# Performance work log

Hardware: AMD Instinct MI355X
Metric: run time of the kernel (lower is better)

Reference implementation:

```python
import jax, jax.numpy as jnp
import numpy as np

EPS = 1e-6        # RMSNorm epsilon (LLaMA convention)
THETA = 10000.0   # RoPE base, from eqx.nn.RotaryPositionalEmbedding(head_dim, 10000)


def rms_norm(x, w):
    # x: [seq, d]; w: [d]
    var = jnp.mean(x * x, axis=-1, keepdims=True)
    return x * jax.lax.rsqrt(var + EPS) * w


def rope(x, offset):
    # x: [seq, heads, head_dim]; half-split (NeoX/equinox) rotation
    seq, _, hd = x.shape
    half = hd // 2
    inv_freq = 1.0 / (THETA ** (jnp.arange(0, half, dtype=jnp.float32) * 2.0 / hd))
    pos = jnp.arange(seq, dtype=jnp.float32) + offset
    ang = jnp.outer(pos, inv_freq)              # [seq, half]
    cos = jnp.cos(ang)[:, None, :]              # [seq, 1, half]
    sin = jnp.sin(ang)[:, None, :]
    x1, x2 = x[..., :half], x[..., half:]
    return jnp.concatenate([x1 * cos - x2 * sin, x2 * cos + x1 * sin], axis=-1)


def setup_inputs() -> dict:
    D, H, HD, S, C = 4096, 32, 128, 1024, 2048
    ks = jax.random.split(jax.random.key(0), 7)
    sc = 1.0 / np.sqrt(D).astype(np.float32)
    return {
        "xs": jax.random.normal(ks[0], (S, D), jnp.float32),
        "cache_k": jax.random.normal(ks[1], (C, H, HD), jnp.float32),
        "cache_v": jax.random.normal(ks[2], (C, H, HD), jnp.float32),
        "norm_w": jnp.ones((D,), jnp.float32),
        "wq": jax.random.normal(ks[3], (D, D), jnp.float32) * sc,
        "wk": jax.random.normal(ks[4], (D, D), jnp.float32) * sc,
        "wv": jax.random.normal(ks[5], (D, D), jnp.float32) * sc,
        "wo": jax.random.normal(ks[6], (D, D), jnp.float32) * sc,
    }


def reference(xs, cache_k, cache_v, norm_w, wq, wk, wv, wo):
    S, D = xs.shape
    C, H, HD = cache_k.shape
    xn = rms_norm(xs, norm_w)                                   # [S, D]
    # eqx.nn.Linear stores weight as [out, in]: y = x @ W.T
    q = rope((xn @ wq.T).reshape(S, H, HD), C)                  # [S, H, HD]
    k_new = rope((xn @ wk.T).reshape(S, H, HD), C)
    v_new = (xn @ wv.T).reshape(S, H, HD)
    k = jnp.concatenate([cache_k, k_new], axis=0)               # [C+S, H, HD]
    v = jnp.concatenate([cache_v, v_new], axis=0)
    scores = jnp.einsum('shd,thd->hst', q, k) / np.float32(np.sqrt(HD))
    # causal with KV cache: query i (global pos C+i) attends keys j <= C+i
    mask = jnp.arange(C + S)[None, :] <= (jnp.arange(S)[:, None] + C)
    scores = jnp.where(mask[None, :, :], scores, jnp.float32(-1e30))
    probs = jax.nn.softmax(scores, axis=-1)                     # [H, S, C+S]
    attn = jnp.einsum('hst,thd->shd', probs, v).reshape(S, D)
    return attn @ wo.T                                          # [S, D]
```

## Files before the change

kernel.cpp:

```cpp
#include <hip/hip_runtime.h>
#include <cmath>

#define S_LEN 1024
#define D_DIM 4096
#define H_NUM 32
#define HD_DIM 128
#define C_LEN 2048
#define T_LEN 3072

using u16 = unsigned short;
typedef __bf16 bf16x8 __attribute__((ext_vector_type(8)));
typedef float f32x4 __attribute__((ext_vector_type(4)));

__device__ __forceinline__ u16 f2bf(float f) {
  unsigned u = __float_as_uint(f);
  return (u16)((u + 0x7FFFu + ((u >> 16) & 1u)) >> 16);
}

__device__ __forceinline__ f32x4 mfma16(bf16x8 a, bf16x8 b, f32x4 c) {
  return __builtin_amdgcn_mfma_f32_16x16x32_bf16(a, b, c, 0, 0, 0);
}

__device__ __forceinline__ void async_cp16(const u16* g, u16* l) {
  __builtin_amdgcn_global_load_lds((const __attribute__((address_space(1))) unsigned int*)g,
                                   (__attribute__((address_space(3))) unsigned int*)l,
                                   16, 0, 0);
}

__global__ __launch_bounds__(256) void cvt_w(const float* __restrict__ src, u16* __restrict__ dst, int n4) {
  int i = blockIdx.x * 256 + threadIdx.x;
  if (i >= n4) return;
  float4 v = ((const float4*)src)[i];
  ushort4 o;
  o.x = f2bf(v.x); o.y = f2bf(v.y); o.z = f2bf(v.z); o.w = f2bf(v.w);
  ((ushort4*)dst)[i] = o;
}

__global__ __launch_bounds__(256) void rmsnorm_k(const float* __restrict__ xs, const float* __restrict__ w,
                                                 u16* __restrict__ xn) {
  int row = blockIdx.x, tid = threadIdx.x;
  const float* xr = xs + (size_t)row * D_DIM;
  float4 xv[4];
  float ss = 0.f;
#pragma unroll
  for (int g = 0; g < 4; ++g) {
    xv[g] = *(const float4*)(xr + g * 1024 + tid * 4);
    ss += xv[g].x * xv[g].x + xv[g].y * xv[g].y + xv[g].z * xv[g].z + xv[g].w * xv[g].w;
  }
#pragma unroll
  for (int m = 1; m < 64; m <<= 1) ss += __shfl_xor(ss, m);
  __shared__ float red[4];
  if ((tid & 63) == 0) red[tid >> 6] = ss;
  __syncthreads();
  float rs = rsqrtf((red[0] + red[1] + red[2] + red[3]) * (1.f / D_DIM) + 1e-6f);
  u16* xo = xn + (size_t)row * D_DIM;
#pragma unroll
  for (int g = 0; g < 4; ++g) {
    float4 wv = *(const float4*)(w + g * 1024 + tid * 4);
    ushort4 o;
    o.x = f2bf(xv[g].x * rs * wv.x);
    o.y = f2bf(xv[g].y * rs * wv.y);
    o.z = f2bf(xv[g].z * rs * wv.z);
    o.w = f2bf(xv[g].w * rs * wv.w);
    *(ushort4*)(xo + g * 1024 + tid * 4) = o;
  }
}

__global__ __launch_bounds__(256) void gemm_bt(const u16* __restrict__ A,
                                               const u16* __restrict__ B0, const u16* __restrict__ B1,
                                               const u16* __restrict__ B2,
                                               float* __restrict__ C0, float* __restrict__ C1,
                                               float* __restrict__ C2) {
  __shared__ u16 As[128 * 32];
  __shared__ u16 Bs[128 * 32];
  int tid = threadIdx.x;
  int wave = tid >> 6, lane = tid & 63, quad = lane >> 4, l15 = lane & 15;
  int wm = wave >> 1, wn = wave & 1;
  int m0 = blockIdx.y * 128, n0 = blockIdx.x * 128;
  int bz = blockIdx.z;
  const u16* Bp = (bz == 0) ? B0 : ((bz == 1) ? B1 : B2);
  float* Cp = (bz == 0) ? C0 : ((bz == 1) ? C1 : C2);

  f32x4 acc[4][4];
  const f32x4 zero4 = {0.f, 0.f, 0.f, 0.f};
#pragma unroll
  for (int mt = 0; mt < 4; ++mt)
#pragma unroll
    for (int nt = 0; nt < 4; ++nt) acc[mt][nt] = zero4;

  int ar = tid >> 2, acol = (tid & 3) * 8;
  const u16* ga0 = A + (size_t)(m0 + ar) * D_DIM + acol;
  const u16* ga1 = A + (size_t)(m0 + 64 + ar) * D_DIM + acol;
  const u16* gb0 = Bp + (size_t)(n0 + ar) * D_DIM + acol;
  const u16* gb1 = Bp + (size_t)(n0 + 64 + ar) * D_DIM + acol;
  u16* la0 = As + (wave << 9);
  u16* la1 = As + 2048 + (wave << 9);
  u16* lb0 = Bs + (wave << 9);
  u16* lb1 = Bs + 2048 + (wave << 9);

  for (int k0 = 0; k0 < D_DIM; k0 += 32) {
    __syncthreads();
    async_cp16(ga0 + k0, la0);
    async_cp16(ga1 + k0, la1);
    async_cp16(gb0 + k0, lb0);
    async_cp16(gb1 + k0, lb1);
    asm volatile("s_waitcnt vmcnt(0)" ::: "memory");
    __syncthreads();
    bf16x8 af[4], bfr[4];
#pragma unroll
    for (int mt = 0; mt < 4; ++mt)
      af[mt] = *(const bf16x8*)(As + (wm * 64 + mt * 16 + l15) * 32 + quad * 8);
#pragma unroll
    for (int nt = 0; nt < 4; ++nt)
      bfr[nt] = *(const bf16x8*)(Bs + (wn * 64 + nt * 16 + l15) * 32 + quad * 8);
#pragma unroll
    for (int mt = 0; mt < 4; ++mt)
#pragma unroll
      for (int nt = 0; nt < 4; ++nt) acc[mt][nt] = mfma16(af[mt], bfr[nt], acc[mt][nt]);
  }
#pragma unroll
  for (int mt = 0; mt < 4; ++mt)
#pragma unroll
    for (int nt = 0; nt < 4; ++nt) {
      int col = n0 + wn * 64 + nt * 16 + l15;
#pragma unroll
      for (int r = 0; r < 4; ++r) {
        int rowm = m0 + wm * 64 + mt * 16 + quad * 4 + r;
        Cp[(size_t)rowm * D_DIM + col] = acc[mt][nt][r];
      }
    }
}

__global__ __launch_bounds__(256) void rope_q_k(const float* __restrict__ qlin, u16* __restrict__ qbf) {
  int idx = blockIdx.x * 256 + threadIdx.x;
  int i = idx & 63, h = (idx >> 6) & 31, s = idx >> 11;
  size_t base = (size_t)s * D_DIM + h * HD_DIM + i;
  float x1 = qlin[base], x2 = qlin[base + 64];
  float invf = expf((float)i * -0.14391156831212790f);
  float ang = (float)(s + C_LEN) * invf;
  float sn, cs;
  sincosf(ang, &sn, &cs);
  const float sc = 0.08838834764831845f;
  qbf[base] = f2bf((x1 * cs - x2 * sn) * sc);
  qbf[base + 64] = f2bf((x2 * cs + x1 * sn) * sc);
}

__global__ __launch_bounds__(256) void rope_k_k(const float* __restrict__ klin, u16* __restrict__ kc) {
  int idx = blockIdx.x * 256 + threadIdx.x;
  int i = idx & 63, h = (idx >> 6) & 31, s = idx >> 11;
  size_t base = (size_t)s * D_DIM + h * HD_DIM + i;
  float x1 = klin[base], x2 = klin[base + 64];
  float invf = expf((float)i * -0.14391156831212790f);
  float ang = (float)(s + C_LEN) * invf;
  float sn, cs;
  sincosf(ang, &sn, &cs);
  size_t ob = ((size_t)h * T_LEN + C_LEN + s) * HD_DIM + i;
  kc[ob] = f2bf(x1 * cs - x2 * sn);
  kc[ob + 64] = f2bf(x2 * cs + x1 * sn);
}

__global__ __launch_bounds__(256) void cvt_ck(const float* __restrict__ ck, u16* __restrict__ kc) {
  int idx = blockIdx.x * 256 + threadIdx.x;
  int flat = idx * 4;
  int c = flat >> 12, h = (flat >> 7) & 31, hd = flat & 127;
  float4 v = *(const float4*)(ck + flat);
  ushort4 o;
  o.x = f2bf(v.x); o.y = f2bf(v.y); o.z = f2bf(v.z); o.w = f2bf(v.w);
  *(ushort4*)(kc + ((size_t)h * T_LEN + c) * HD_DIM + hd) = o;
}

__global__ __launch_bounds__(256) void trans_v(const float* __restrict__ src, u16* __restrict__ vt, int tofs) {
  int h = blockIdx.z, d0 = blockIdx.x * 64, r0 = blockIdx.y * 64;
  __shared__ float tile[64][65];
  int tid = threadIdx.x;
  int rr = tid >> 4, c4 = (tid & 15) * 4;
#pragma unroll
  for (int p = 0; p < 4; ++p) {
    int r = p * 16 + rr;
    float4 v = *(const float4*)(src + (size_t)(r0 + r) * D_DIM + h * HD_DIM + d0 + c4);
    tile[r][c4] = v.x; tile[r][c4 + 1] = v.y; tile[r][c4 + 2] = v.z; tile[r][c4 + 3] = v.w;
  }
  __syncthreads();
#pragma unroll
  for (int p = 0; p < 4; ++p) {
    int dl = p * 16 + rr;
    ushort4 o;
    o.x = f2bf(tile[c4 + 0][dl]);
    o.y = f2bf(tile[c4 + 1][dl]);
    o.z = f2bf(tile[c4 + 2][dl]);
    o.w = f2bf(tile[c4 + 3][dl]);
    *(ushort4*)(vt + ((size_t)h * HD_DIM + d0 + dl) * T_LEN + tofs + r0 + c4) = o;
  }
}

__global__ __launch_bounds__(256) void attn_k(const u16* __restrict__ qb, const u16* __restrict__ kc,
                                              const u16* __restrict__ vt, u16* __restrict__ ob) {
  int qt = blockIdx.x, h = blockIdx.y;
  int tid = threadIdx.x, wave = tid >> 6, lane = tid & 63, quad = lane >> 4, l15 = lane & 15;
  __shared__ u16 Ks[64 * 136];
  __shared__ u16 Vs[128 * 72];
  __shared__ u16 Ps[4 * 16 * 72];

  int qrow = qt * 64 + wave * 16 + l15;
  bf16x8 qf[4];
#pragma unroll
  for (int kt = 0; kt < 4; ++kt)
    qf[kt] = *(const bf16x8*)(qb + (size_t)qrow * D_DIM + h * HD_DIM + kt * 32 + quad * 8);

  f32x4 O[8];
  const f32x4 zero4 = {0.f, 0.f, 0.f, 0.f};
#pragma unroll
  for (int i = 0; i < 8; ++i) O[i] = zero4;
  float mrun[4] = {-INFINITY, -INFINITY, -INFINITY, -INFINITY};
  float lrun[4] = {0.f, 0.f, 0.f, 0.f};

  int ktl = tid >> 2, kcc = (tid & 3) * 32;
  int vd = tid >> 1, vtt = (tid & 1) * 32;
  const u16* kg = kc + ((size_t)h * T_LEN + ktl) * HD_DIM + kcc;
  const u16* vg = vt + ((size_t)h * HD_DIM + vd) * T_LEN + vtt;
  u16* kl = Ks + ktl * 136 + kcc;
  u16* vl = Vs + vd * 72 + vtt;

  int nkb = 33 + qt;
  for (int kb = 0; kb < nkb; ++kb) {
    __syncthreads();
#pragma unroll
    for (int u = 0; u < 4; ++u)
      *(bf16x8*)(kl + u * 8) = *(const bf16x8*)(kg + (size_t)kb * 64 * HD_DIM + u * 8);
#pragma unroll
    for (int u = 0; u < 4; ++u)
      *(bf16x8*)(vl + u * 8) = *(const bf16x8*)(vg + (size_t)kb * 64 + u * 8);
    __syncthreads();

    f32x4 sc4[4];
#pragma unroll
    for (int nt = 0; nt < 4; ++nt) {
      f32x4 s = zero4;
#pragma unroll
      for (int kt = 0; kt < 4; ++kt) {
        bf16x8 bv = *(const bf16x8*)(Ks + (nt * 16 + l15) * 136 + kt * 32 + quad * 8);
        s = mfma16(qf[kt], bv, s);
      }
      sc4[nt] = s;
    }
    if (kb == nkb - 1) {
#pragma unroll
      for (int nt = 0; nt < 4; ++nt) {
        int t = kb * 64 + nt * 16 + l15;
#pragma unroll
        for (int r = 0; r < 4; ++r) {
          int srow = qt * 64 + wave * 16 + quad * 4 + r;
          if (t > C_LEN + srow) sc4[nt][r] = -INFINITY;
        }
      }
    }
    float alpha4[4];
#pragma unroll
    for (int r = 0; r < 4; ++r) {
      float mx = fmaxf(fmaxf(sc4[0][r], sc4[1][r]), fmaxf(sc4[2][r], sc4[3][r]));
      mx = fmaxf(mx, __shfl_xor(mx, 1));
      mx = fmaxf(mx, __shfl_xor(mx, 2));
      mx = fmaxf(mx, __shfl_xor(mx, 4));
      mx = fmaxf(mx, __shfl_xor(mx, 8));
      float nm = fmaxf(mrun[r], mx);
      float al = __expf(mrun[r] - nm);
      float ps = 0.f;
#pragma unroll
      for (int nt = 0; nt < 4; ++nt) {
        float p = __expf(sc4[nt][r] - nm);
        sc4[nt][r] = p;
        ps += p;
      }
      ps += __shfl_xor(ps, 1);
      ps += __shfl_xor(ps, 2);
      ps += __shfl_xor(ps, 4);
      ps += __shfl_xor(ps, 8);
      lrun[r] = lrun[r] * al + ps;
      mrun[r] = nm;
      alpha4[r] = al;
    }
#pragma unroll
    for (int i = 0; i < 8; ++i)
#pragma unroll
      for (int r = 0; r < 4; ++r) O[i][r] *= alpha4[r];

    u16* pw = Ps + wave * (16 * 72);
#pragma unroll
    for (int nt = 0; nt < 4; ++nt)
#pragma unroll
      for (int r = 0; r < 4; ++r)
        pw[(quad * 4 + r) * 72 + nt * 16 + l15] = f2bf(sc4[nt][r]);
    asm volatile("s_waitcnt lgkmcnt(0)" ::: "memory");

#pragma unroll
    for (int kt2 = 0; kt2 < 2; ++kt2) {
      bf16x8 af = *(const bf16x8*)(pw + l15 * 72 + kt2 * 32 + quad * 8);
#pragma unroll
      for (int nt2 = 0; nt2 < 8; ++nt2) {
        bf16x8 bv = *(const bf16x8*)(Vs + (nt2 * 16 + l15) * 72 + kt2 * 32 + quad * 8);
        O[nt2] = mfma16(af, bv, O[nt2]);
      }
    }
  }
  float inv[4];
#pragma unroll
  for (int r = 0; r < 4; ++r) inv[r] = 1.f / lrun[r];
#pragma unroll
  for (int nt2 = 0; nt2 < 8; ++nt2)
#pragma unroll
    for (int r = 0; r < 4; ++r) {
      int srow = qt * 64 + wave * 16 + quad * 4 + r;
      ob[(size_t)srow * D_DIM + h * HD_DIM + nt2 * 16 + l15] = f2bf(O[nt2][r] * inv[r]);
    }
}

extern "C" void kernel_launch(void* const* d_in, const int* in_sizes, int n_in,
                              void* d_out, int out_size, void* d_ws, size_t ws_size,
                              hipStream_t stream) {
  const float* xs = (const float*)d_in[0];
  const float* cache_k = (const float*)d_in[1];
  const float* cache_v = (const float*)d_in[2];
  const float* norm_w = (const float*)d_in[3];
  const float* wq = (const float*)d_in[4];
  const float* wk = (const float*)d_in[5];
  const float* wv = (const float*)d_in[6];
  const float* wo = (const float*)d_in[7];
  float* out = (float*)d_out;

  char* ws = (char*)d_ws;
  size_t off = 0;
  auto take = [&](size_t b) -> void* {
    char* p = ws + off;
    off += (b + 255) & ~(size_t)255;
    return (void*)p;
  };
  u16* wq_bf = (u16*)take((size_t)D_DIM * D_DIM * 2);
  u16* wk_bf = (u16*)take((size_t)D_DIM * D_DIM * 2);
  u16* wv_bf = (u16*)take((size_t)D_DIM * D_DIM * 2);
  u16* wo_bf = (u16*)take((size_t)D_DIM * D_DIM * 2);
  u16* xn_bf = (u16*)take((size_t)S_LEN * D_DIM * 2);
  float* q_lin = (float*)take((size_t)S_LEN * D_DIM * 4);
  float* k_lin = (float*)take((size_t)S_LEN * D_DIM * 4);
  float* v_lin = (float*)take((size_t)S_LEN * D_DIM * 4);
  u16* q_bf = (u16*)take((size_t)S_LEN * D_DIM * 2);
  u16* k_cat = (u16*)take((size_t)H_NUM * T_LEN * HD_DIM * 2);
  u16* v_t = (u16*)take((size_t)H_NUM * T_LEN * HD_DIM * 2);
  u16* attn_bf = (u16*)take((size_t)S_LEN * D_DIM * 2);

  int n4w = D_DIM * D_DIM / 4;
  cvt_w<<<n4w / 256, 256, 0, stream>>>(wq, wq_bf, n4w);
  cvt_w<<<n4w / 256, 256, 0, stream>>>(wk, wk_bf, n4w);
  cvt_w<<<n4w / 256, 256, 0, stream>>>(wv, wv_bf, n4w);
  cvt_w<<<n4w / 256, 256, 0, stream>>>(wo, wo_bf, n4w);
  rmsnorm_k<<<S_LEN, 256, 0, stream>>>(xs, norm_w, xn_bf);
  gemm_bt<<<dim3(32, 8, 3), 256, 0, stream>>>(xn_bf, wq_bf, wk_bf, wv_bf, q_lin, k_lin, v_lin);
  rope_q_k<<<(S_LEN * H_NUM * 64) / 256, 256, 0, stream>>>(q_lin, q_bf);
  rope_k_k<<<(S_LEN * H_NUM * 64) / 256, 256, 0, stream>>>(k_lin, k_cat);
  cvt_ck<<<(C_LEN * H_NUM * HD_DIM / 4) / 256, 256, 0, stream>>>(cache_k, k_cat);
  trans_v<<<dim3(2, C_LEN / 64, H_NUM), 256, 0, stream>>>(cache_v, v_t, 0);
  trans_v<<<dim3(2, S_LEN / 64, H_NUM), 256, 0, stream>>>(v_lin, v_t, C_LEN);
  attn_k<<<dim3(16, 32), 256, 0, stream>>>(q_bf, k_cat, v_t, attn_bf);
  gemm_bt<<<dim3(32, 8, 1), 256, 0, stream>>>(attn_bf, wo_bf, wo_bf, wo_bf, out, out, out);
}
```

Before: 808.9 us.

## Double-buffer attention K/V with async loads, deepen GEMM k-step, merge small kernels

The attention kernel now stages K and V tiles into double-buffered shared memory with async global-to-LDS copies and XOR-swizzled layouts, so the next tile's loads overlap compute. The P scratch now reuses the current K buffer behind an extra barrier. The GEMM loads two 32-wide k-slices per barrier, halving the sync count. Weight conversion, RoPE and V transposition are each merged into a single launch to cut launch overhead. In exchange, LDS use and register pressure rise, and the shared-buffer aliasing adds synchronization subtlety.

```diff
diff --git a/kernel.cpp b/kernel.cpp
--- a/kernel.cpp
+++ b/kernel.cpp
@@ -27,13 +27,16 @@
                                    16, 0, 0);
 }
 
-__global__ __launch_bounds__(256) void cvt_w(const float* __restrict__ src, u16* __restrict__ dst, int n4) {
+__global__ __launch_bounds__(256) void cvt_w4(const float* __restrict__ w0, const float* __restrict__ w1,
+                                              const float* __restrict__ w2, const float* __restrict__ w3,
+                                              u16* __restrict__ dst) {
+  int y = blockIdx.y;
+  const float* src = (y == 0) ? w0 : (y == 1) ? w1 : (y == 2) ? w2 : w3;
   int i = blockIdx.x * 256 + threadIdx.x;
-  if (i >= n4) return;
   float4 v = ((const float4*)src)[i];
   ushort4 o;
   o.x = f2bf(v.x); o.y = f2bf(v.y); o.z = f2bf(v.z); o.w = f2bf(v.w);
-  ((ushort4*)dst)[i] = o;
+  ((ushort4*)(dst + (size_t)y * D_DIM * D_DIM))[i] = o;
 }
 
 __global__ __launch_bounds__(256) void rmsnorm_k(const float* __restrict__ xs, const float* __restrict__ w,
@@ -71,8 +74,8 @@
                                                const u16* __restrict__ B2,
                                                float* __restrict__ C0, float* __restrict__ C1,
                                                float* __restrict__ C2) {
-  __shared__ u16 As[128 * 32];
-  __shared__ u16 Bs[128 * 32];
+  __shared__ u16 As[2 * 128 * 32];
+  __shared__ u16 Bs[2 * 128 * 32];
   int tid = threadIdx.x;
   int wave = tid >> 6, lane = tid & 63, quad = lane >> 4, l15 = lane & 15;
   int wm = wave >> 1, wn = wave & 1;
@@ -93,30 +96,32 @@
   const u16* ga1 = A + (size_t)(m0 + 64 + ar) * D_DIM + acol;
   const u16* gb0 = Bp + (size_t)(n0 + ar) * D_DIM + acol;
   const u16* gb1 = Bp + (size_t)(n0 + 64 + ar) * D_DIM + acol;
-  u16* la0 = As + (wave << 9);
-  u16* la1 = As + 2048 + (wave << 9);
-  u16* lb0 = Bs + (wave << 9);
-  u16* lb1 = Bs + 2048 + (wave << 9);
-
-  for (int k0 = 0; k0 < D_DIM; k0 += 32) {
+
+  for (int k0 = 0; k0 < D_DIM; k0 += 64) {
     __syncthreads();
-    async_cp16(ga0 + k0, la0);
-    async_cp16(ga1 + k0, la1);
-    async_cp16(gb0 + k0, lb0);
-    async_cp16(gb1 + k0, lb1);
+#pragma unroll
+    for (int hf = 0; hf < 2; ++hf) {
+      async_cp16(ga0 + k0 + hf * 32, As + hf * 4096 + (wave << 9));
+      async_cp16(ga1 + k0 + hf * 32, As + hf * 4096 + 2048 + (wave << 9));
+      async_cp16(gb0 + k0 + hf * 32, Bs + hf * 4096 + (wave << 9));
+      async_cp16(gb1 + k0 + hf * 32, Bs + hf * 4096 + 2048 + (wave << 9));
+    }
     asm volatile("s_waitcnt vmcnt(0)" ::: "memory");
     __syncthreads();
-    bf16x8 af[4], bfr[4];
-#pragma unroll
-    for (int mt = 0; mt < 4; ++mt)
-      af[mt] = *(const bf16x8*)(As + (wm * 64 + mt * 16 + l15) * 32 + quad * 8);
-#pragma unroll
-    for (int nt = 0; nt < 4; ++nt)
-      bfr[nt] = *(const bf16x8*)(Bs + (wn * 64 + nt * 16 + l15) * 32 + quad * 8);
-#pragma unroll
-    for (int mt = 0; mt < 4; ++mt)
-#pragma unroll
-      for (int nt = 0; nt < 4; ++nt) acc[mt][nt] = mfma16(af[mt], bfr[nt], acc[mt][nt]);
+#pragma unroll
+    for (int hf = 0; hf < 2; ++hf) {
+      bf16x8 af[4], bfr[4];
+#pragma unroll
+      for (int mt = 0; mt < 4; ++mt)
+        af[mt] = *(const bf16x8*)(As + hf * 4096 + (wm * 64 + mt * 16 + l15) * 32 + quad * 8);
+#pragma unroll
+      for (int nt = 0; nt < 4; ++nt)
+        bfr[nt] = *(const bf16x8*)(Bs + hf * 4096 + (wn * 64 + nt * 16 + l15) * 32 + quad * 8);
+#pragma unroll
+      for (int mt = 0; mt < 4; ++mt)
+#pragma unroll
+        for (int nt = 0; nt < 4; ++nt) acc[mt][nt] = mfma16(af[mt], bfr[nt], acc[mt][nt]);
+    }
   }
 #pragma unroll
   for (int mt = 0; mt < 4; ++mt)
@@ -131,32 +136,27 @@
     }
 }
 
-__global__ __launch_bounds__(256) void rope_q_k(const float* __restrict__ qlin, u16* __restrict__ qbf) {
+__global__ __launch_bounds__(256) void rope_qk(const float* __restrict__ qlin, const float* __restrict__ klin,
+                                               u16* __restrict__ qbf, u16* __restrict__ kc) {
+  int part = blockIdx.y;
   int idx = blockIdx.x * 256 + threadIdx.x;
   int i = idx & 63, h = (idx >> 6) & 31, s = idx >> 11;
   size_t base = (size_t)s * D_DIM + h * HD_DIM + i;
-  float x1 = qlin[base], x2 = qlin[base + 64];
   float invf = expf((float)i * -0.14391156831212790f);
   float ang = (float)(s + C_LEN) * invf;
   float sn, cs;
   sincosf(ang, &sn, &cs);
-  const float sc = 0.08838834764831845f;
-  qbf[base] = f2bf((x1 * cs - x2 * sn) * sc);
-  qbf[base + 64] = f2bf((x2 * cs + x1 * sn) * sc);
-}
-
-__global__ __launch_bounds__(256) void rope_k_k(const float* __restrict__ klin, u16* __restrict__ kc) {
-  int idx = blockIdx.x * 256 + threadIdx.x;
-  int i = idx & 63, h = (idx >> 6) & 31, s = idx >> 11;
-  size_t base = (size_t)s * D_DIM + h * HD_DIM + i;
-  float x1 = klin[base], x2 = klin[base + 64];
-  float invf = expf((float)i * -0.14391156831212790f);
-  float ang = (float)(s + C_LEN) * invf;
-  float sn, cs;
-  sincosf(ang, &sn, &cs);
-  size_t ob = ((size_t)h * T_LEN + C_LEN + s) * HD_DIM + i;
-  kc[ob] = f2bf(x1 * cs - x2 * sn);
-  kc[ob + 64] = f2bf(x2 * cs + x1 * sn);
+  if (part == 0) {
+    float x1 = qlin[base], x2 = qlin[base + 64];
+    const float sc = 0.08838834764831845f;
+    qbf[base] = f2bf((x1 * cs - x2 * sn) * sc);
+    qbf[base + 64] = f2bf((x2 * cs + x1 * sn) * sc);
+  } else {
+    float x1 = klin[base], x2 = klin[base + 64];
+    size_t ob = ((size_t)h * T_LEN + C_LEN + s) * HD_DIM + i;
+    kc[ob] = f2bf(x1 * cs - x2 * sn);
+    kc[ob + 64] = f2bf(x2 * cs + x1 * sn);
+  }
 }
 
 __global__ __launch_bounds__(256) void cvt_ck(const float* __restrict__ ck, u16* __restrict__ kc) {
@@ -169,15 +169,19 @@
   *(ushort4*)(kc + ((size_t)h * T_LEN + c) * HD_DIM + hd) = o;
 }
 
-__global__ __launch_bounds__(256) void trans_v(const float* __restrict__ src, u16* __restrict__ vt, int tofs) {
+__global__ __launch_bounds__(256) void trans_v2(const float* __restrict__ cv, const float* __restrict__ vl,
+                                                u16* __restrict__ vt) {
   int h = blockIdx.z, d0 = blockIdx.x * 64, r0 = blockIdx.y * 64;
+  const float* src;
+  int srow;
+  if (r0 < C_LEN) { src = cv; srow = r0; } else { src = vl; srow = r0 - C_LEN; }
   __shared__ float tile[64][65];
   int tid = threadIdx.x;
   int rr = tid >> 4, c4 = (tid & 15) * 4;
 #pragma unroll
   for (int p = 0; p < 4; ++p) {
     int r = p * 16 + rr;
-    float4 v = *(const float4*)(src + (size_t)(r0 + r) * D_DIM + h * HD_DIM + d0 + c4);
+    float4 v = *(const float4*)(src + (size_t)(srow + r) * D_DIM + h * HD_DIM + d0 + c4);
     tile[r][c4] = v.x; tile[r][c4 + 1] = v.y; tile[r][c4 + 2] = v.z; tile[r][c4 + 3] = v.w;
   }
   __syncthreads();
@@ -189,17 +193,16 @@
     o.y = f2bf(tile[c4 + 1][dl]);
     o.z = f2bf(tile[c4 + 2][dl]);
     o.w = f2bf(tile[c4 + 3][dl]);
-    *(ushort4*)(vt + ((size_t)h * HD_DIM + d0 + dl) * T_LEN + tofs + r0 + c4) = o;
+    *(ushort4*)(vt + ((size_t)h * HD_DIM + d0 + dl) * T_LEN + r0 + c4) = o;
   }
 }
 
 __global__ __launch_bounds__(256) void attn_k(const u16* __restrict__ qb, const u16* __restrict__ kc,
                                               const u16* __restrict__ vt, u16* __restrict__ ob) {
+  __shared__ u16 Kb[2][8192];
+  __shared__ u16 Vb[2][8192];
   int qt = blockIdx.x, h = blockIdx.y;
   int tid = threadIdx.x, wave = tid >> 6, lane = tid & 63, quad = lane >> 4, l15 = lane & 15;
-  __shared__ u16 Ks[64 * 136];
-  __shared__ u16 Vs[128 * 72];
-  __shared__ u16 Ps[4 * 16 * 72];
 
   int qrow = qt * 64 + wave * 16 + l15;
   bf16x8 qf[4];
@@ -214,23 +217,29 @@
   float mrun[4] = {-INFINITY, -INFINITY, -INFINITY, -INFINITY};
   float lrun[4] = {0.f, 0.f, 0.f, 0.f};
 
-  int ktl = tid >> 2, kcc = (tid & 3) * 32;
-  int vd = tid >> 1, vtt = (tid & 1) * 32;
-  const u16* kg = kc + ((size_t)h * T_LEN + ktl) * HD_DIM + kcc;
-  const u16* vg = vt + ((size_t)h * HD_DIM + vd) * T_LEN + vtt;
-  u16* kl = Ks + ktl * 136 + kcc;
-  u16* vl = Vs + vd * 72 + vtt;
-
+  int kr = tid >> 4;
+  int kcg = (tid & 15) ^ (kr & 15);
+  int vr = tid >> 3;
+  int vcg = (tid & 7) ^ (vr & 7);
+  const u16* kg = kc + ((size_t)h * T_LEN + kr) * HD_DIM + kcg * 8;
+  const u16* vg = vt + ((size_t)h * HD_DIM + vr) * T_LEN + vcg * 8;
+
+  auto stage = [&](int kb, int buf) {
+    const u16* kp = kg + (size_t)kb * 64 * HD_DIM;
+    const u16* vp = vg + (size_t)kb * 64;
+#pragma unroll
+    for (int p = 0; p < 4; ++p) async_cp16(kp + p * 16 * HD_DIM, &Kb[buf][p * 2048 + (wave << 9)]);
+#pragma unroll
+    for (int p = 0; p < 4; ++p) async_cp16(vp + (size_t)p * 32 * T_LEN, &Vb[buf][p * 2048 + (wave << 9)]);
+  };
+
+  stage(0, 0);
   int nkb = 33 + qt;
   for (int kb = 0; kb < nkb; ++kb) {
+    int cur = kb & 1;
+    asm volatile("s_waitcnt vmcnt(0)" ::: "memory");
     __syncthreads();
-#pragma unroll
-    for (int u = 0; u < 4; ++u)
-      *(bf16x8*)(kl + u * 8) = *(const bf16x8*)(kg + (size_t)kb * 64 * HD_DIM + u * 8);
-#pragma unroll
-    for (int u = 0; u < 4; ++u)
-      *(bf16x8*)(vl + u * 8) = *(const bf16x8*)(vg + (size_t)kb * 64 + u * 8);
-    __syncthreads();
+    if (kb + 1 < nkb) stage(kb + 1, cur ^ 1);
 
     f32x4 sc4[4];
 #pragma unroll
@@ -238,7 +247,8 @@
       f32x4 s = zero4;
 #pragma unroll
       for (int kt = 0; kt < 4; ++kt) {
-        bf16x8 bv = *(const bf16x8*)(Ks + (nt * 16 + l15) * 136 + kt * 32 + quad * 8);
+        int row = nt * 16 + l15;
+        bf16x8 bv = *(const bf16x8*)&Kb[cur][row * 128 + (((kt * 4 + quad) ^ l15) * 8)];
         s = mfma16(qf[kt], bv, s);
       }
       sc4[nt] = s;
@@ -284,7 +294,9 @@
 #pragma unroll
       for (int r = 0; r < 4; ++r) O[i][r] *= alpha4[r];
 
-    u16* pw = Ps + wave * (16 * 72);
+    asm volatile("s_waitcnt lgkmcnt(0)\n\ts_barrier" ::: "memory");
+
+    u16* pw = &Kb[cur][wave * 1152];
 #pragma unroll
     for (int nt = 0; nt < 4; ++nt)
 #pragma unroll
@@ -297,7 +309,8 @@
       bf16x8 af = *(const bf16x8*)(pw + l15 * 72 + kt2 * 32 + quad * 8);
 #pragma unroll
       for (int nt2 = 0; nt2 < 8; ++nt2) {
-        bf16x8 bv = *(const bf16x8*)(Vs + (nt2 * 16 + l15) * 72 + kt2 * 32 + quad * 8);
+        int row = nt2 * 16 + l15;
+        bf16x8 bv = *(const bf16x8*)&Vb[cur][row * 64 + (((kt2 * 4 + quad) ^ (l15 & 7)) * 8)];
         O[nt2] = mfma16(af, bv, O[nt2]);
       }
     }
@@ -334,10 +347,11 @@
     off += (b + 255) & ~(size_t)255;
     return (void*)p;
   };
-  u16* wq_bf = (u16*)take((size_t)D_DIM * D_DIM * 2);
-  u16* wk_bf = (u16*)take((size_t)D_DIM * D_DIM * 2);
-  u16* wv_bf = (u16*)take((size_t)D_DIM * D_DIM * 2);
-  u16* wo_bf = (u16*)take((size_t)D_DIM * D_DIM * 2);
+  u16* w_bf = (u16*)take((size_t)4 * D_DIM * D_DIM * 2);
+  u16* wq_bf = w_bf;
+  u16* wk_bf = w_bf + (size_t)D_DIM * D_DIM;
+  u16* wv_bf = w_bf + (size_t)2 * D_DIM * D_DIM;
+  u16* wo_bf = w_bf + (size_t)3 * D_DIM * D_DIM;
   u16* xn_bf = (u16*)take((size_t)S_LEN * D_DIM * 2);
   float* q_lin = (float*)take((size_t)S_LEN * D_DIM * 4);
   float* k_lin = (float*)take((size_t)S_LEN * D_DIM * 4);
@@ -347,18 +361,12 @@
   u16* v_t = (u16*)take((size_t)H_NUM * T_LEN * HD_DIM * 2);
   u16* attn_bf = (u16*)take((size_t)S_LEN * D_DIM * 2);
 
-  int n4w = D_DIM * D_DIM / 4;
-  cvt_w<<<n4w / 256, 256, 0, stream>>>(wq, wq_bf, n4w);
-  cvt_w<<<n4w / 256, 256, 0, stream>>>(wk, wk_bf, n4w);
-  cvt_w<<<n4w / 256, 256, 0, stream>>>(wv, wv_bf, n4w);
-  cvt_w<<<n4w / 256, 256, 0, stream>>>(wo, wo_bf, n4w);
+  cvt_w4<<<dim3(D_DIM * D_DIM / 4 / 256, 4), 256, 0, stream>>>(wq, wk, wv, wo, w_bf);
   rmsnorm_k<<<S_LEN, 256, 0, stream>>>(xs, norm_w, xn_bf);
   gemm_bt<<<dim3(32, 8, 3), 256, 0, stream>>>(xn_bf, wq_bf, wk_bf, wv_bf, q_lin, k_lin, v_lin);
-  rope_q_k<<<(S_LEN * H_NUM * 64) / 256, 256, 0, stream>>>(q_lin, q_bf);
-  rope_k_k<<<(S_LEN * H_NUM * 64) / 256, 256, 0, stream>>>(k_lin, k_cat);
+  rope_qk<<<dim3((S_LEN * H_NUM * 64) / 256, 2), 256, 0, stream>>>(q_lin, k_lin, q_bf, k_cat);
   cvt_ck<<<(C_LEN * H_NUM * HD_DIM / 4) / 256, 256, 0, stream>>>(cache_k, k_cat);
-  trans_v<<<dim3(2, C_LEN / 64, H_NUM), 256, 0, stream>>>(cache_v, v_t, 0);
-  trans_v<<<dim3(2, S_LEN / 64, H_NUM), 256, 0, stream>>>(v_lin, v_t, C_LEN);
+  trans_v2<<<dim3(2, T_LEN / 64, H_NUM), 256, 0, stream>>>(cache_v, v_lin, v_t);
   attn_k<<<dim3(16, 32), 256, 0, stream>>>(q_bf, k_cat, v_t, attn_bf);
   gemm_bt<<<dim3(32, 8, 1), 256, 0, stream>>>(attn_bf, wo_bf, wo_bf, wo_bf, out, out, out);
 }
```

After: 734.4 us. 1.1x faster.
